# Performance work log

Hardware: AMD Instinct MI355X
Metric: run time of the kernel (lower is better)

## Reference

```python
import jax, jax.numpy as jnp
import numpy as np

N_CONTENT = 100000
N_USER = 100000
N_EDGES = 1600000
D_CONTENT = 256
D_USER = 128
HIDDEN = 128
OUT = 64


def setup_inputs() -> dict:
    key = jax.random.key(0)
    ks = jax.random.split(key, 12)
    s = lambda d: 1.0 / np.sqrt(d)
    return {
        "x_content": jax.random.normal(ks[0], (N_CONTENT, D_CONTENT), jnp.float32),
        "x_user": jax.random.normal(ks[1], (N_USER, D_USER), jnp.float32),
        # edge_index[0] = source (user) ids, edge_index[1] = destination (content) ids
        "edge_index": jax.random.randint(ks[2], (2, N_EDGES), 0, N_CONTENT, jnp.int64),
        # per-node-type input projections
        "Wc": jax.random.normal(ks[3], (D_CONTENT, HIDDEN), jnp.float32) * s(D_CONTENT),
        "bc": jnp.zeros((HIDDEN,), jnp.float32),
        "Wu": jax.random.normal(ks[4], (D_USER, HIDDEN), jnp.float32) * s(D_USER),
        "bu": jnp.zeros((HIDDEN,), jnp.float32),
        # SAGEConv: W_l applied to aggregated neighbor features (with bias),
        # W_r applied to root/self features (no bias, per PyG default)
        "Wl": jax.random.normal(ks[5], (HIDDEN, HIDDEN), jnp.float32) * s(HIDDEN),
        "bl": jnp.zeros((HIDDEN,), jnp.float32),
        "Wr": jax.random.normal(ks[6], (HIDDEN, HIDDEN), jnp.float32) * s(HIDDEN),
        # final output projection on content nodes
        "Wo": jax.random.normal(ks[7], (HIDDEN, OUT), jnp.float32) * s(HIDDEN),
        "bo": jnp.zeros((OUT,), jnp.float32),
    }


def reference(x_content, x_user, edge_index, Wc, bc, Wu, bu, Wl, bl, Wr, Wo, bo):
    # Per-node-type linear + relu
    h_c = jax.nn.relu(x_content @ Wc + bc)  # [Nc, H]
    h_u = jax.nn.relu(x_user @ Wu + bu)      # [Nu, H]

    src, dst = edge_index[0], edge_index[1]
    # SAGEConv mean aggregation: gather user features along edges, scatter-mean to content
    msg = h_u[src]                                              # [E, H] gather
    agg = jax.ops.segment_sum(msg, dst, num_segments=N_CONTENT) # [Nc, H]
    cnt = jax.ops.segment_sum(jnp.ones((msg.shape[0],), msg.dtype), dst,
                              num_segments=N_CONTENT)
    mean = agg / jnp.maximum(cnt, 1.0)[:, None]                 # 0 for isolated nodes

    h = mean @ Wl + bl + h_c @ Wr                               # SAGE combine
    return h @ Wo + bo                                          # [Nc, OUT]
```

## Files before the change

### kernel.cpp

```cpp
#include <hip/hip_runtime.h>
#include <hip/hip_bf16.h>

#define NC 100000
#define NU 100000
#define NE 1600000
#define DC 256
#define DU 128
#define HID 128
#define OUTD 64

#define BSHIFT 9
#define BRANGE 512
#define NBUCK ((NC + BRANGE - 1) / BRANGE)
#define BCAP 10240
#define EPB 8192
#define ABLK ((NE + EPB - 1) / EPB)

#define NBT_C ((NC + 63) / 64)
#define NBT_U ((NU + 63) / 64)

typedef __attribute__((ext_vector_type(8))) short bf16x8;
typedef __attribute__((ext_vector_type(4))) float f32x4;

__device__ inline unsigned short f2b(float f) {
    unsigned int u = __float_as_uint(f);
    u += 0x7fffu + ((u >> 16) & 1u);
    return (unsigned short)(u >> 16);
}

__global__ void prep_kernel(const float* __restrict__ Wl, const float* __restrict__ bl,
                            const float* __restrict__ Wr, const float* __restrict__ Wo,
                            const float* __restrict__ bo,
                            __hip_bfloat16* __restrict__ Wlo_p,
                            __hip_bfloat16* __restrict__ Wro_p,
                            float* __restrict__ b2) {
    const int k = blockIdx.x;
    const int f = threadIdx.x;
    float a0 = 0.f, a1 = 0.f;
    for (int m = 0; m < HID; ++m) {
        float wo = Wo[m * OUTD + f];
        a0 = fmaf(Wl[k * HID + m], wo, a0);
        a1 = fmaf(Wr[k * HID + m], wo, a1);
    }
    const int wv = f >> 4, l16 = f & 15;
    const int ks = k >> 5, quad = (k >> 3) & 3, e = k & 7;
    const int idx = (((wv * 4 + ks) * 64) + quad * 16 + l16) * 8 + e;
    Wlo_p[idx] = __float2bfloat16(a0);
    Wro_p[idx] = __float2bfloat16(a1);
    if (k == 0) {
        float s = bo[f];
        for (int m = 0; m < HID; ++m) s = fmaf(bl[m], Wo[m * OUTD + f], s);
        b2[f] = s;
    }
}

__global__ void pack_w(const float* __restrict__ W, __hip_bfloat16* __restrict__ Wp,
                       int K) {
    int i = blockIdx.x * blockDim.x + threadIdx.x;
    int total = K * HID;
    if (i >= total) return;
    int j = i % HID, k = i / HID;
    int nks = K >> 5;
    int idx = (((j >> 4) * nks + (k >> 5)) * 64 + ((k >> 3) & 3) * 16 + (j & 15)) * 8 +
              (k & 7);
    Wp[idx] = __float2bfloat16(W[k * HID + j]);
}

template <int DIN, bool BF16OUT>
__device__ __forceinline__ void gemm_path(const float* __restrict__ x,
                                          const __hip_bfloat16* __restrict__ W1p,
                                          const float* __restrict__ b1,
                                          const __hip_bfloat16* __restrict__ W2p,
                                          const float* __restrict__ bias2,
                                          void* __restrict__ outp, int nrows, int tile,
                                          short* __restrict__ smem) {
    constexpr int NKS = DIN / 32;
    constexpr int SA = DIN + 8;
    constexpr int SH = HID + 8;
    short* a_s = smem;
    short* h_s = smem + 64 * (DC + 8);

    const int t = threadIdx.x;
    const int w = t >> 6, lane = t & 63;
    const int quad = lane >> 4, l16 = lane & 15;
    const int base = tile * 64;

    bf16x8 b1f[2][NKS];
#pragma unroll
    for (int ntl = 0; ntl < 2; ++ntl)
#pragma unroll
        for (int ks = 0; ks < NKS; ++ks)
            b1f[ntl][ks] =
                *(const bf16x8*)&W1p[(size_t)(((2 * w + ntl) * NKS + ks) * 64 + lane) * 8];

    constexpr int CPR = DIN / 8;
    constexpr int NCH = 64 * CPR / 256;
#pragma unroll
    for (int hh = 0; hh < NCH / 4; ++hh) {
        float4 va[4][2];
#pragma unroll
        for (int i = 0; i < 4; ++i) {
            int c = (hh * 4 + i) * 256 + t;
            int r = c / CPR, cc = c % CPR;
            int rc = min(base + r, nrows - 1);
            const float4* p = (const float4*)(x + (size_t)rc * DIN + cc * 8);
            va[i][0] = p[0];
            va[i][1] = p[1];
        }
#pragma unroll
        for (int i = 0; i < 4; ++i) {
            int c = (hh * 4 + i) * 256 + t;
            int r = c / CPR, cc = c % CPR;
            bf16x8 a;
            a[0] = (short)f2b(va[i][0].x); a[1] = (short)f2b(va[i][0].y);
            a[2] = (short)f2b(va[i][0].z); a[3] = (short)f2b(va[i][0].w);
            a[4] = (short)f2b(va[i][1].x); a[5] = (short)f2b(va[i][1].y);
            a[6] = (short)f2b(va[i][1].z); a[7] = (short)f2b(va[i][1].w);
            *(bf16x8*)&a_s[r * SA + cc * 8] = a;
        }
    }
    __syncthreads();

    float bb1[2];
    bb1[0] = b1[w * 32 + l16];
    bb1[1] = b1[w * 32 + 16 + l16];
#pragma unroll
    for (int rg = 0; rg < 4; ++rg) {
        bf16x8 af[NKS];
#pragma unroll
        for (int ks = 0; ks < NKS; ++ks)
            af[ks] = *(const bf16x8*)&a_s[(rg * 16 + l16) * SA + ks * 32 + quad * 8];
        f32x4 acc0 = (f32x4){0.f, 0.f, 0.f, 0.f};
        f32x4 acc1 = (f32x4){0.f, 0.f, 0.f, 0.f};
#pragma unroll
        for (int ks = 0; ks < NKS; ++ks) {
            acc0 = __builtin_amdgcn_mfma_f32_16x16x32_bf16(af[ks], b1f[0][ks], acc0, 0, 0, 0);
            acc1 = __builtin_amdgcn_mfma_f32_16x16x32_bf16(af[ks], b1f[1][ks], acc1, 0, 0, 0);
        }
#pragma unroll
        for (int r = 0; r < 4; ++r) {
            float v0 = fmaxf(acc0[r] + bb1[0], 0.f);
            float v1 = fmaxf(acc1[r] + bb1[1], 0.f);
            int row = rg * 16 + quad * 4 + r;
            h_s[row * SH + w * 32 + l16] = (short)f2b(v0);
            h_s[row * SH + w * 32 + 16 + l16] = (short)f2b(v1);
        }
    }
    __syncthreads();

    bf16x8 b2f[HID / 32];
#pragma unroll
    for (int ks = 0; ks < HID / 32; ++ks)
        b2f[ks] = *(const bf16x8*)&W2p[(size_t)((w * 4 + ks) * 64 + lane) * 8];
    float bb2 = BF16OUT ? 0.f : bias2[w * 16 + l16];
#pragma unroll
    for (int rg = 0; rg < 4; ++rg) {
        f32x4 acc = (f32x4){0.f, 0.f, 0.f, 0.f};
#pragma unroll
        for (int ks = 0; ks < HID / 32; ++ks) {
            bf16x8 a = *(const bf16x8*)&h_s[(rg * 16 + l16) * SH + ks * 32 + quad * 8];
            acc = __builtin_amdgcn_mfma_f32_16x16x32_bf16(a, b2f[ks], acc, 0, 0, 0);
        }
#pragma unroll
        for (int r = 0; r < 4; ++r) {
            int rr = base + rg * 16 + quad * 4 + r;
            if (rr < nrows) {
                if (BF16OUT)
                    ((unsigned short*)outp)[(size_t)rr * OUTD + w * 16 + l16] = f2b(acc[r]);
                else
                    ((float*)outp)[(size_t)rr * OUTD + w * 16 + l16] = acc[r] + bb2;
            }
        }
    }
}

__global__ void __launch_bounds__(256, 3) dual_gemm(
    const float* __restrict__ xc, const __hip_bfloat16* __restrict__ Wc_p,
    const float* __restrict__ bc, const __hip_bfloat16* __restrict__ Wro_p,
    const float* __restrict__ b2, float* __restrict__ out,
    const float* __restrict__ xu, const __hip_bfloat16* __restrict__ Wu_p,
    const float* __restrict__ bu, const __hip_bfloat16* __restrict__ Wlo_p,
    unsigned short* __restrict__ pu) {
    __shared__ __align__(16) short smem[64 * (DC + 8) + 64 * (HID + 8)];
    int b = blockIdx.x;
    if (b < NBT_C)
        gemm_path<DC, false>(xc, Wc_p, bc, Wro_p, b2, out, NC, b, smem);
    else
        gemm_path<DU, true>(xu, Wu_p, bu, Wlo_p, nullptr, pu, NU, b - NBT_C, smem);
}

__global__ void __launch_bounds__(256) bucket_a(const int* __restrict__ src,
                                                const int* __restrict__ dst,
                                                int* __restrict__ gcur,
                                                unsigned int* __restrict__ bke) {
    __shared__ unsigned int pk[EPB];
    __shared__ int hist[NBUCK];
    __shared__ int lbase[NBUCK];
    __shared__ int lcur[NBUCK];
    __shared__ int gb[NBUCK];
    __shared__ int ts[256];
    const int t = threadIdx.x;
    const int base = blockIdx.x * EPB;
    for (int i = t; i < NBUCK; i += 256) hist[i] = 0;
    __syncthreads();
#pragma unroll
    for (int k = 0; k < EPB / 256; ++k) {
        int e = base + k * 256 + t;
        if (e < NE) atomicAdd(&hist[dst[e] >> BSHIFT], 1);
    }
    __syncthreads();
    int h = (t < NBUCK) ? hist[t] : 0;
    ts[t] = h;
    __syncthreads();
    for (int d = 1; d < 256; d <<= 1) {
        int x = (t >= d) ? ts[t - d] : 0;
        __syncthreads();
        ts[t] += x;
        __syncthreads();
    }
    if (t < NBUCK) {
        int ex = ts[t] - h;
        lbase[t] = ex;
        lcur[t] = ex;
        gb[t] = atomicAdd(&gcur[t], h);
    }
    __syncthreads();
#pragma unroll
    for (int k = 0; k < EPB / 256; ++k) {
        int e = base + k * 256 + t;
        if (e < NE) {
            int s = src[e], d = dst[e];
            int b = d >> BSHIFT;
            int p = atomicAdd(&lcur[b], 1);
            pk[p] = ((unsigned int)s << BSHIFT) | (unsigned int)(d & (BRANGE - 1));
        }
    }
    __syncthreads();
    const int wv = t >> 6, ln = t & 63;
    for (int b = wv; b < NBUCK; b += 4) {
        int s0 = lbase[b], c = hist[b], g0 = gb[b];
        for (int j = ln; j < c; j += 64) {
            int pos = g0 + j;
            if (pos < BCAP) bke[(size_t)b * BCAP + pos] = pk[s0 + j];
        }
    }
}

__global__ void scan_mid(const int* __restrict__ gcur, int* __restrict__ gbase,
                         int* __restrict__ off) {
    __shared__ int ts[256];
    int t = threadIdx.x;
    int h = (t < NBUCK) ? gcur[t] : 0;
    ts[t] = h;
    __syncthreads();
    for (int d = 1; d < 256; d <<= 1) {
        int x = (t >= d) ? ts[t - d] : 0;
        __syncthreads();
        ts[t] += x;
        __syncthreads();
    }
    if (t < NBUCK) gbase[t] = ts[t] - h;
    if (t == 0) { gbase[NBUCK] = NE; off[NC] = NE; }
}

__global__ void __launch_bounds__(256) bucket_b(const int* __restrict__ gcur,
                                                const int* __restrict__ gbase,
                                                const unsigned int* __restrict__ bke,
                                                int* __restrict__ off,
                                                int* __restrict__ ssrc) {
    __shared__ unsigned int pk[BCAP];
    __shared__ int hist[BRANGE];
    __shared__ int hb[BRANGE];
    __shared__ int cur[BRANGE];
    __shared__ int ts[256];
    const int t = threadIdx.x;
    const int b = blockIdx.x;
    const int n = min(gcur[b], BCAP);
    const int g0 = gbase[b];
    for (int i = t; i < n; i += 256) pk[i] = bke[(size_t)b * BCAP + i];
    for (int i = t; i < BRANGE; i += 256) hist[i] = 0;
    __syncthreads();
    for (int i = t; i < n; i += 256) atomicAdd(&hist[pk[i] & (BRANGE - 1)], 1);
    __syncthreads();
    int a0 = hist[2 * t], a1 = hist[2 * t + 1];
    int s = a0 + a1;
    ts[t] = s;
    __syncthreads();
    for (int d = 1; d < 256; d <<= 1) {
        int x = (t >= d) ? ts[t - d] : 0;
        __syncthreads();
        ts[t] += x;
        __syncthreads();
    }
    int ex = ts[t] - s;
    hb[2 * t] = ex;
    hb[2 * t + 1] = ex + a0;
    __syncthreads();
    for (int i = t; i < BRANGE; i += 256) {
        int node = b * BRANGE + i;
        cur[i] = g0 + hb[i];
        if (node < NC) off[node] = g0 + hb[i];
    }
    __syncthreads();
    for (int i = t; i < n; i += 256) {
        unsigned int v = pk[i];
        int p = atomicAdd(&cur[v & (BRANGE - 1)], 1);
        ssrc[p] = (int)(v >> BSHIFT);
    }
}

__global__ void __launch_bounds__(256) gather_agg(const int* __restrict__ ssrc,
                                                  const int* __restrict__ off,
                                                  const unsigned int* __restrict__ pu,
                                                  float* __restrict__ out) {
    int node = blockIdx.x * 4 + (threadIdx.x >> 6);
    if (node >= NC) return;
    int lane = threadIdx.x & 63;
    int g = lane >> 3;
    int f8 = lane & 7;
    int e0 = off[node], e1 = off[node + 1];
    float acc[8] = {0.f, 0.f, 0.f, 0.f, 0.f, 0.f, 0.f, 0.f};
    for (int e = e0 + g; e < e1; e += 8) {
        int s = ssrc[e];
        uint4 v = ((const uint4*)pu)[(size_t)s * 8 + f8];
        acc[0] += __uint_as_float(v.x << 16);
        acc[1] += __uint_as_float(v.x & 0xffff0000u);
        acc[2] += __uint_as_float(v.y << 16);
        acc[3] += __uint_as_float(v.y & 0xffff0000u);
        acc[4] += __uint_as_float(v.z << 16);
        acc[5] += __uint_as_float(v.z & 0xffff0000u);
        acc[6] += __uint_as_float(v.w << 16);
        acc[7] += __uint_as_float(v.w & 0xffff0000u);
    }
#pragma unroll
    for (int m = 8; m <= 32; m <<= 1) {
#pragma unroll
        for (int j = 0; j < 8; ++j) acc[j] += __shfl_xor(acc[j], m, 64);
    }
    if (g == 0) {
        float inv = 1.0f / (float)max(e1 - e0, 1);
        float4* po = (float4*)(out + (size_t)node * OUTD + f8 * 8);
        float4 o0 = po[0], o1 = po[1];
        o0.x += acc[0] * inv; o0.y += acc[1] * inv;
        o0.z += acc[2] * inv; o0.w += acc[3] * inv;
        o1.x += acc[4] * inv; o1.y += acc[5] * inv;
        o1.z += acc[6] * inv; o1.w += acc[7] * inv;
        po[0] = o0; po[1] = o1;
    }
}

extern "C" void kernel_launch(void* const* d_in, const int* in_sizes, int n_in,
                              void* d_out, int out_size, void* d_ws, size_t ws_size,
                              hipStream_t stream) {
    const float* xc = (const float*)d_in[0];
    const float* xu = (const float*)d_in[1];
    const int*   ei = (const int*)d_in[2];
    const float* Wc = (const float*)d_in[3];
    const float* bc = (const float*)d_in[4];
    const float* Wu = (const float*)d_in[5];
    const float* bu = (const float*)d_in[6];
    const float* Wl = (const float*)d_in[7];
    const float* bl = (const float*)d_in[8];
    const float* Wr = (const float*)d_in[9];
    const float* Wo = (const float*)d_in[10];
    const float* bo = (const float*)d_in[11];
    float* out = (float*)d_out;

    const int* esrc = ei;
    const int* edst = ei + NE;

    unsigned short* pu = (unsigned short*)d_ws;
    int* ssrc  = (int*)(pu + (size_t)NU * OUTD);
    unsigned int* bke = (unsigned int*)(ssrc + NE);
    int* gcur  = (int*)(bke + (size_t)NBUCK * BCAP);
    int* gbase = gcur + NBUCK;
    int* off   = gcur + 400;
    float* b2  = (float*)(off + NC + 4);
    __hip_bfloat16* Wlo_p = (__hip_bfloat16*)(b2 + OUTD);
    __hip_bfloat16* Wro_p = Wlo_p + OUTD * HID;
    __hip_bfloat16* Wu_p  = Wro_p + OUTD * HID;
    __hip_bfloat16* Wc_p  = Wu_p + HID * DU;

    hipMemsetAsync(gcur, 0, NBUCK * sizeof(int), stream);

    prep_kernel<<<HID, OUTD, 0, stream>>>(Wl, bl, Wr, Wo, bo, Wlo_p, Wro_p, b2);
    pack_w<<<(DU * HID + 255) / 256, 256, 0, stream>>>(Wu, Wu_p, DU);
    pack_w<<<(DC * HID + 255) / 256, 256, 0, stream>>>(Wc, Wc_p, DC);

    dual_gemm<<<NBT_C + NBT_U, 256, 0, stream>>>(xc, Wc_p, bc, Wro_p, b2, out,
                                                 xu, Wu_p, bu, Wlo_p, pu);

    bucket_a<<<ABLK, 256, 0, stream>>>(esrc, edst, gcur, bke);
    scan_mid<<<1, 256, 0, stream>>>(gcur, gbase, off);
    bucket_b<<<NBUCK, 256, 0, stream>>>(gcur, gbase, bke, off, ssrc);
    gather_agg<<<(NC + 3) / 4, 256, 0, stream>>>(ssrc, off, (const unsigned int*)pu, out);
}
```

Before: 340.6 us.

## Make dual GEMM persistent with register prefetch of next tile

The dual GEMM kernel becomes persistent: a fixed grid of 342 content blocks and 170 user blocks loops over 64-row tiles, and each block loads the next tile's fp32 input into registers while computing the current one. Weight fragments and biases are loaded once per block instead of once per tile. This aims to hide global-load latency and cut per-block setup and launch cost. The prefetch buffer raises register pressure, so launch bounds drop from 3 to 2 waves' worth of occupancy, which reduces latency hiding across blocks.

```diff
diff --git a/kernel.cpp b/kernel.cpp
--- a/kernel.cpp
+++ b/kernel.cpp
@@ -18,6 +18,9 @@
 
 #define NBT_C ((NC + 63) / 64)
 #define NBT_U ((NU + 63) / 64)
+
+#define NBC 342
+#define NBU 170
 
 typedef __attribute__((ext_vector_type(8))) short bf16x8;
 typedef __attribute__((ext_vector_type(4))) float f32x4;
@@ -72,18 +75,22 @@
                                           const float* __restrict__ b1,
                                           const __hip_bfloat16* __restrict__ W2p,
                                           const float* __restrict__ bias2,
-                                          void* __restrict__ outp, int nrows, int tile,
+                                          void* __restrict__ outp, int nrows,
+                                          int ntiles, int blk, int nblk,
                                           short* __restrict__ smem) {
     constexpr int NKS = DIN / 32;
     constexpr int SA = DIN + 8;
     constexpr int SH = HID + 8;
+    constexpr int CPR = DIN / 8;
+    constexpr int NCH = 64 * CPR / 256;
+    constexpr int RSTEP = 256 / CPR;
     short* a_s = smem;
     short* h_s = smem + 64 * (DC + 8);
 
     const int t = threadIdx.x;
     const int w = t >> 6, lane = t & 63;
     const int quad = lane >> 4, l16 = lane & 15;
-    const int base = tile * 64;
+    const int r0 = t / CPR, c0 = t % CPR;
 
     bf16x8 b1f[2][NKS];
 #pragma unroll
@@ -92,89 +99,88 @@
         for (int ks = 0; ks < NKS; ++ks)
             b1f[ntl][ks] =
                 *(const bf16x8*)&W1p[(size_t)(((2 * w + ntl) * NKS + ks) * 64 + lane) * 8];
-
-    constexpr int CPR = DIN / 8;
-    constexpr int NCH = 64 * CPR / 256;
-#pragma unroll
-    for (int hh = 0; hh < NCH / 4; ++hh) {
-        float4 va[4][2];
-#pragma unroll
-        for (int i = 0; i < 4; ++i) {
-            int c = (hh * 4 + i) * 256 + t;
-            int r = c / CPR, cc = c % CPR;
-            int rc = min(base + r, nrows - 1);
-            const float4* p = (const float4*)(x + (size_t)rc * DIN + cc * 8);
-            va[i][0] = p[0];
-            va[i][1] = p[1];
-        }
-#pragma unroll
-        for (int i = 0; i < 4; ++i) {
-            int c = (hh * 4 + i) * 256 + t;
-            int r = c / CPR, cc = c % CPR;
-            bf16x8 a;
-            a[0] = (short)f2b(va[i][0].x); a[1] = (short)f2b(va[i][0].y);
-            a[2] = (short)f2b(va[i][0].z); a[3] = (short)f2b(va[i][0].w);
-            a[4] = (short)f2b(va[i][1].x); a[5] = (short)f2b(va[i][1].y);
-            a[6] = (short)f2b(va[i][1].z); a[7] = (short)f2b(va[i][1].w);
-            *(bf16x8*)&a_s[r * SA + cc * 8] = a;
-        }
-    }
-    __syncthreads();
-
-    float bb1[2];
-    bb1[0] = b1[w * 32 + l16];
-    bb1[1] = b1[w * 32 + 16 + l16];
-#pragma unroll
-    for (int rg = 0; rg < 4; ++rg) {
-        bf16x8 af[NKS];
-#pragma unroll
-        for (int ks = 0; ks < NKS; ++ks)
-            af[ks] = *(const bf16x8*)&a_s[(rg * 16 + l16) * SA + ks * 32 + quad * 8];
-        f32x4 acc0 = (f32x4){0.f, 0.f, 0.f, 0.f};
-        f32x4 acc1 = (f32x4){0.f, 0.f, 0.f, 0.f};
-#pragma unroll
-        for (int ks = 0; ks < NKS; ++ks) {
-            acc0 = __builtin_amdgcn_mfma_f32_16x16x32_bf16(af[ks], b1f[0][ks], acc0, 0, 0, 0);
-            acc1 = __builtin_amdgcn_mfma_f32_16x16x32_bf16(af[ks], b1f[1][ks], acc1, 0, 0, 0);
-        }
-#pragma unroll
-        for (int r = 0; r < 4; ++r) {
-            float v0 = fmaxf(acc0[r] + bb1[0], 0.f);
-            float v1 = fmaxf(acc1[r] + bb1[1], 0.f);
-            int row = rg * 16 + quad * 4 + r;
-            h_s[row * SH + w * 32 + l16] = (short)f2b(v0);
-            h_s[row * SH + w * 32 + 16 + l16] = (short)f2b(v1);
-        }
-    }
-    __syncthreads();
-
     bf16x8 b2f[HID / 32];
 #pragma unroll
     for (int ks = 0; ks < HID / 32; ++ks)
         b2f[ks] = *(const bf16x8*)&W2p[(size_t)((w * 4 + ks) * 64 + lane) * 8];
-    float bb2 = BF16OUT ? 0.f : bias2[w * 16 + l16];
-#pragma unroll
-    for (int rg = 0; rg < 4; ++rg) {
-        f32x4 acc = (f32x4){0.f, 0.f, 0.f, 0.f};
-#pragma unroll
-        for (int ks = 0; ks < HID / 32; ++ks) {
-            bf16x8 a = *(const bf16x8*)&h_s[(rg * 16 + l16) * SH + ks * 32 + quad * 8];
-            acc = __builtin_amdgcn_mfma_f32_16x16x32_bf16(a, b2f[ks], acc, 0, 0, 0);
-        }
-#pragma unroll
-        for (int r = 0; r < 4; ++r) {
-            int rr = base + rg * 16 + quad * 4 + r;
-            if (rr < nrows) {
-                if (BF16OUT)
-                    ((unsigned short*)outp)[(size_t)rr * OUTD + w * 16 + l16] = f2b(acc[r]);
-                else
-                    ((float*)outp)[(size_t)rr * OUTD + w * 16 + l16] = acc[r] + bb2;
+    const float bb1_0 = b1[w * 32 + l16];
+    const float bb1_1 = b1[w * 32 + 16 + l16];
+    const float bb2 = BF16OUT ? 0.f : bias2[w * 16 + l16];
+
+    float4 va[NCH][2];
+
+    auto load_tile = [&](int tile) {
+#pragma unroll
+        for (int k = 0; k < NCH; ++k) {
+            int rc = min(tile * 64 + r0 + k * RSTEP, nrows - 1);
+            const float4* p = (const float4*)(x + (size_t)rc * DIN + c0 * 8);
+            va[k][0] = p[0];
+            va[k][1] = p[1];
+        }
+    };
+
+    load_tile(blk);
+
+    for (int tile = blk; tile < ntiles; tile += nblk) {
+#pragma unroll
+        for (int k = 0; k < NCH; ++k) {
+            bf16x8 a;
+            a[0] = (short)f2b(va[k][0].x); a[1] = (short)f2b(va[k][0].y);
+            a[2] = (short)f2b(va[k][0].z); a[3] = (short)f2b(va[k][0].w);
+            a[4] = (short)f2b(va[k][1].x); a[5] = (short)f2b(va[k][1].y);
+            a[6] = (short)f2b(va[k][1].z); a[7] = (short)f2b(va[k][1].w);
+            *(bf16x8*)&a_s[(r0 + k * RSTEP) * SA + c0 * 8] = a;
+        }
+        int tn = tile + nblk;
+        if (tn < ntiles) load_tile(tn);
+        __syncthreads();
+
+#pragma unroll
+        for (int rg = 0; rg < 4; ++rg) {
+            bf16x8 af[NKS];
+#pragma unroll
+            for (int ks = 0; ks < NKS; ++ks)
+                af[ks] = *(const bf16x8*)&a_s[(rg * 16 + l16) * SA + ks * 32 + quad * 8];
+            f32x4 acc0 = (f32x4){0.f, 0.f, 0.f, 0.f};
+            f32x4 acc1 = (f32x4){0.f, 0.f, 0.f, 0.f};
+#pragma unroll
+            for (int ks = 0; ks < NKS; ++ks) {
+                acc0 = __builtin_amdgcn_mfma_f32_16x16x32_bf16(af[ks], b1f[0][ks], acc0, 0, 0, 0);
+                acc1 = __builtin_amdgcn_mfma_f32_16x16x32_bf16(af[ks], b1f[1][ks], acc1, 0, 0, 0);
             }
-        }
-    }
-}
-
-__global__ void __launch_bounds__(256, 3) dual_gemm(
+#pragma unroll
+            for (int r = 0; r < 4; ++r) {
+                int row = rg * 16 + quad * 4 + r;
+                h_s[row * SH + w * 32 + l16] = (short)f2b(fmaxf(acc0[r] + bb1_0, 0.f));
+                h_s[row * SH + w * 32 + 16 + l16] = (short)f2b(fmaxf(acc1[r] + bb1_1, 0.f));
+            }
+        }
+        __syncthreads();
+
+        const int base = tile * 64;
+#pragma unroll
+        for (int rg = 0; rg < 4; ++rg) {
+            f32x4 acc = (f32x4){0.f, 0.f, 0.f, 0.f};
+#pragma unroll
+            for (int ks = 0; ks < HID / 32; ++ks) {
+                bf16x8 a = *(const bf16x8*)&h_s[(rg * 16 + l16) * SH + ks * 32 + quad * 8];
+                acc = __builtin_amdgcn_mfma_f32_16x16x32_bf16(a, b2f[ks], acc, 0, 0, 0);
+            }
+#pragma unroll
+            for (int r = 0; r < 4; ++r) {
+                int rr = base + rg * 16 + quad * 4 + r;
+                if (rr < nrows) {
+                    if (BF16OUT)
+                        ((unsigned short*)outp)[(size_t)rr * OUTD + w * 16 + l16] = f2b(acc[r]);
+                    else
+                        ((float*)outp)[(size_t)rr * OUTD + w * 16 + l16] = acc[r] + bb2;
+                }
+            }
+        }
+    }
+}
+
+__global__ void __launch_bounds__(256, 2) dual_gemm(
     const float* __restrict__ xc, const __hip_bfloat16* __restrict__ Wc_p,
     const float* __restrict__ bc, const __hip_bfloat16* __restrict__ Wro_p,
     const float* __restrict__ b2, float* __restrict__ out,
@@ -183,10 +189,10 @@
     unsigned short* __restrict__ pu) {
     __shared__ __align__(16) short smem[64 * (DC + 8) + 64 * (HID + 8)];
     int b = blockIdx.x;
-    if (b < NBT_C)
-        gemm_path<DC, false>(xc, Wc_p, bc, Wro_p, b2, out, NC, b, smem);
+    if (b < NBC)
+        gemm_path<DC, false>(xc, Wc_p, bc, Wro_p, b2, out, NC, NBT_C, b, NBC, smem);
     else
-        gemm_path<DU, true>(xu, Wu_p, bu, Wlo_p, nullptr, pu, NU, b - NBT_C, smem);
+        gemm_path<DU, true>(xu, Wu_p, bu, Wlo_p, nullptr, pu, NU, NBT_U, b - NBC, NBU, smem);
 }
 
 __global__ void __launch_bounds__(256) bucket_a(const int* __restrict__ src,
@@ -387,8 +393,8 @@
     pack_w<<<(DU * HID + 255) / 256, 256, 0, stream>>>(Wu, Wu_p, DU);
     pack_w<<<(DC * HID + 255) / 256, 256, 0, stream>>>(Wc, Wc_p, DC);
 
-    dual_gemm<<<NBT_C + NBT_U, 256, 0, stream>>>(xc, Wc_p, bc, Wro_p, b2, out,
-                                                 xu, Wu_p, bu, Wlo_p, pu);
+    dual_gemm<<<NBC + NBU, 256, 0, stream>>>(xc, Wc_p, bc, Wro_p, b2, out,
+                                             xu, Wu_p, bu, Wlo_p, pu);
 
     bucket_a<<<ABLK, 256, 0, stream>>>(esrc, edst, gcur, bke);
     scan_mid<<<1, 256, 0, stream>>>(gcur, gbase, off);
```

New measurement: 344.6 us. Within noise of the previous version (+1.2%).
